# Kernel optimization log

Measured on AMD Instinct MI355X. Metric: run time of the kernel, lower is better.

## Reference

```python
import jax, jax.numpy as jnp
import numpy as np

RWKV_EPS = 1e-20
RWKV_K_CLAMP = 60.0

N, C, E = 25000, 128, 400000


def setup_inputs() -> dict:
    key = jax.random.key(0)
    ks = jax.random.split(key, 14)
    return {
        "x": jax.random.normal(ks[0], (N, C), jnp.float32),
        "prev_x": jax.random.normal(ks[1], (N, C), jnp.float32),
        "ah": jax.random.uniform(ks[2], (E, C), jnp.float32),
        "bh": jax.random.uniform(ks[3], (E, C), jnp.float32),
        "Wk": jax.random.normal(ks[4], (C, C), jnp.float32) / np.sqrt(C),
        "Wv": jax.random.normal(ks[5], (C, C), jnp.float32) / np.sqrt(C),
        "Wr": jax.random.normal(ks[6], (C, C), jnp.float32) / np.sqrt(C),
        "Wo": jax.random.normal(ks[7], (C, C), jnp.float32) / np.sqrt(C),
        "time_mix_k": jax.random.uniform(ks[8], (1, C), jnp.float32),
        "time_mix_v": jax.random.uniform(ks[9], (1, C), jnp.float32),
        "time_mix_r": jax.random.uniform(ks[10], (1, C), jnp.float32),
        "time_w": jax.random.uniform(ks[11], (1, C), jnp.float32),
        "s": jax.random.randint(ks[12], (E,), 0, N, jnp.int64),
        "t": jax.random.randint(ks[13], (E,), 0, N, jnp.int64),
        "i": 5,
        "T": 16,
    }


def reference(x, prev_x, ah, bh, Wk, Wv, Wr, Wo,
              time_mix_k, time_mix_v, time_mix_r, time_w, s, t, i, T):
    # time-shift mixing on node features [N, C]
    xk = x * time_mix_k + prev_x * (1.0 - time_mix_k)
    xv = x * time_mix_v + prev_x * (1.0 - time_mix_v)
    xr = x * time_mix_r + prev_x * (1.0 - time_mix_r)
    # torch Linear: y = x @ W.T ; gather to edges [E, C]
    k = (xk @ Wk.T)[s]
    v = (xv @ Wv.T)[t]
    r = jax.nn.sigmoid((xr @ Wr.T)[s])
    k = jnp.exp(jnp.minimum(k, RWKV_K_CLAMP))
    w = jnp.exp(-(T - i - 1) * time_w)  # [1, C] decay
    kv = w * (k * v)
    a = ah + kv
    b = bh + k
    wkv = a / (b + RWKV_EPS)
    out = (r * wkv) @ Wo.T  # [E, C]
    return out
```

## Files before the change

### kernel.cpp

```cpp
#include <hip/hip_runtime.h>

#define CDIM 128

typedef short short8 __attribute__((ext_vector_type(8)));
typedef float f32x4 __attribute__((ext_vector_type(4)));

__device__ __forceinline__ unsigned short f2bf(float f) {
  unsigned int u = __builtin_bit_cast(unsigned int, f);
  u += 0x7fffu + ((u >> 16) & 1u);
  return (unsigned short)(u >> 16);
}
__device__ __forceinline__ float bf2f(unsigned short b) {
  return __builtin_bit_cast(float, (unsigned int)b << 16);
}
__device__ __forceinline__ void split_bf(float v, unsigned short& h,
                                         unsigned short& l) {
  h = f2bf(v);
  l = f2bf(v - bf2f(h));
}


__global__ __launch_bounds__(256) void pack_w(
    const float* __restrict__ Wk, const float* __restrict__ Wv,
    const float* __restrict__ Wr, const float* __restrict__ Wo,
    unsigned short* __restrict__ wf) {
  const int f = blockIdx.x * 256 + threadIdx.x;
  const int m = f >> 12;
  const int idx = (f & 4095) * 4;
  const int e0 = idx & 7;
  const int l = (idx >> 3) & 63;
  const int nt = (idx >> 9) & 7;
  const int kt = idx >> 12;
  const float* W = (m == 0) ? Wk : (m == 1) ? Wv : (m == 2) ? Wr : Wo;
  const int j = nt * 16 + (l & 15);
  const int c = kt * 32 + (l >> 4) * 8 + e0;
  float4 v = *(const float4*)(W + j * CDIM + c);
  ushort4 h, lo;
  split_bf(v.x, h.x, lo.x);
  split_bf(v.y, h.y, lo.y);
  split_bf(v.z, h.z, lo.z);
  split_bf(v.w, h.w, lo.w);
  unsigned short* base = wf + m * 32768;
  *(ushort4*)(base + idx) = h;
  *(ushort4*)(base + 16384 + idx) = lo;
}


#define MFMA __builtin_amdgcn_mfma_f32_16x16x32_bf16

__device__ __forceinline__ void stage_w(unsigned short* Wl,
                                        const unsigned short* wsrc, int t) {
  const float4* src = (const float4*)wsrc;
  float4* dst = (float4*)Wl;
#pragma unroll
  for (int it = 0; it < 16; ++it) dst[it * 256 + t] = src[it * 256 + t];
}

__device__ __forceinline__ void mfma_all(const unsigned short* Wl,
                                         const short8 ahi[2][4],
                                         const short8 alo[2][4],
                                         f32x4 acc[2][8], int lane) {
#pragma unroll
  for (int kt = 0; kt < 4; ++kt) {
#pragma unroll
    for (int nt = 0; nt < 8; ++nt) {
      const int fo = ((kt * 8 + nt) * 64 + lane) * 8;
      short8 bhi = *(const short8*)(Wl + fo);
      short8 blo = *(const short8*)(Wl + 16384 + fo);
      acc[0][nt] = MFMA(ahi[0][kt], bhi, acc[0][nt], 0, 0, 0);
      acc[1][nt] = MFMA(ahi[1][kt], bhi, acc[1][nt], 0, 0, 0);
      acc[0][nt] = MFMA(alo[0][kt], bhi, acc[0][nt], 0, 0, 0);
      acc[1][nt] = MFMA(alo[1][kt], bhi, acc[1][nt], 0, 0, 0);
      acc[0][nt] = MFMA(ahi[0][kt], blo, acc[0][nt], 0, 0, 0);
      acc[1][nt] = MFMA(ahi[1][kt], blo, acc[1][nt], 0, 0, 0);
    }
  }
}

__global__ __launch_bounds__(256, 2) void node_mfma(
    const float* __restrict__ x, const float* __restrict__ px,
    const float* __restrict__ tmk, const float* __restrict__ tmv,
    const float* __restrict__ tmr, const unsigned short* __restrict__ wf,
    float* __restrict__ kvr, int N) {
  __shared__ alignas(16) unsigned short Wl[32768];
  const int t = threadIdx.x;
  const int m = blockIdx.y;
  stage_w(Wl, wf + m * 32768, t);
  const float* __restrict__ tm = (m == 0) ? tmk : (m == 1) ? tmv : tmr;
  const int lane = t & 63;
  const int w = t >> 6;
  const int lr = lane & 15, lg = lane >> 4;
  const int rbase = blockIdx.x * 128 + w * 32;

  short8 ahi[2][4], alo[2][4];
#pragma unroll
  for (int kt = 0; kt < 4; ++kt) {
    const int c0 = kt * 32 + lg * 8;
    float tmx[8];
    *(float4*)tmx = *(const float4*)(tm + c0);
    *(float4*)(tmx + 4) = *(const float4*)(tm + c0 + 4);
#pragma unroll
    for (int mt = 0; mt < 2; ++mt) {
      const int r = rbase + mt * 16 + lr;
      float xa[8], pa[8];
      if (r < N) {
        const float* xp = x + (size_t)r * CDIM + c0;
        const float* pp = px + (size_t)r * CDIM + c0;
        *(float4*)xa = *(const float4*)xp;
        *(float4*)(xa + 4) = *(const float4*)(xp + 4);
        *(float4*)pa = *(const float4*)pp;
        *(float4*)(pa + 4) = *(const float4*)(pp + 4);
      } else {
#pragma unroll
        for (int q = 0; q < 8; ++q) { xa[q] = 0.f; pa[q] = 0.f; }
      }
      short8 hv, lv;
#pragma unroll
      for (int q = 0; q < 8; ++q) {
        float xm = pa[q] + tmx[q] * (xa[q] - pa[q]);
        unsigned short hb, lb;
        split_bf(xm, hb, lb);
        hv[q] = (short)hb;
        lv[q] = (short)lb;
      }
      ahi[mt][kt] = hv;
      alo[mt][kt] = lv;
    }
  }
  __syncthreads();

  f32x4 acc[2][8];
#pragma unroll
  for (int mt = 0; mt < 2; ++mt)
#pragma unroll
    for (int nt = 0; nt < 8; ++nt) {
      f32x4 z = {0.f, 0.f, 0.f, 0.f};
      acc[mt][nt] = z;
    }
  mfma_all(Wl, ahi, alo, acc, lane);

  float* outb = kvr + (size_t)m * N * CDIM;
#pragma unroll
  for (int mt = 0; mt < 2; ++mt) {
    const int rb = rbase + mt * 16 + lg * 4;
#pragma unroll
    for (int nt = 0; nt < 8; ++nt) {
#pragma unroll
      for (int g = 0; g < 4; ++g) {
        const int r = rb + g;
        if (r < N) outb[(size_t)r * CDIM + nt * 16 + lr] = acc[mt][nt][g];
      }
    }
  }
}

__global__ __launch_bounds__(256, 2) void edge_mfma(
    const float* __restrict__ ah, const float* __restrict__ bh,
    const int* __restrict__ sidx, const int* __restrict__ tidx,
    const int* __restrict__ ip, const int* __restrict__ Tp,
    const float* __restrict__ time_w, const unsigned short* __restrict__ wf,
    const float* __restrict__ kvr, float* __restrict__ out, int N) {
  __shared__ alignas(16) unsigned short Wl[32768];
  const int t = threadIdx.x;
  stage_w(Wl, wf + 3 * 32768, t);
  const int lane = t & 63;
  const int w = t >> 6;
  const int lr = lane & 15, lg = lane >> 4;
  const size_t rbase = (size_t)blockIdx.x * 128 + w * 32;
  const float* __restrict__ Kb = kvr;
  const float* __restrict__ Vb = kvr + (size_t)N * CDIM;
  const float* __restrict__ Rb = kvr + 2 * (size_t)N * CDIM;
  const float dec = -(float)(Tp[0] - ip[0] - 1);

  const size_t er0 = rbase + lr, er1 = rbase + 16 + lr;
  const int s0 = sidx[er0], t0 = tidx[er0];
  const int s1 = sidx[er1], t1 = tidx[er1];

  short8 ahi[2][4], alo[2][4];
#pragma unroll
  for (int kt = 0; kt < 4; ++kt) {
    const int c0 = kt * 32 + lg * 8;
    float tww[8], wd[8];
    *(float4*)tww = *(const float4*)(time_w + c0);
    *(float4*)(tww + 4) = *(const float4*)(time_w + c0 + 4);
#pragma unroll
    for (int q = 0; q < 8; ++q) wd[q] = __expf(dec * tww[q]);
#pragma unroll
    for (int mt = 0; mt < 2; ++mt) {
      const size_t r = mt ? er1 : er0;
      const int se = mt ? s1 : s0;
      const int te = mt ? t1 : t0;
      float aa[8], bb[8], kk[8], vv[8], rr[8];
      {
        const float* p = ah + r * CDIM + c0;
        *(float4*)aa = *(const float4*)p;
        *(float4*)(aa + 4) = *(const float4*)(p + 4);
      }
      {
        const float* p = bh + r * CDIM + c0;
        *(float4*)bb = *(const float4*)p;
        *(float4*)(bb + 4) = *(const float4*)(p + 4);
      }
      {
        const float* p = Kb + (size_t)se * CDIM + c0;
        *(float4*)kk = *(const float4*)p;
        *(float4*)(kk + 4) = *(const float4*)(p + 4);
      }
      {
        const float* p = Vb + (size_t)te * CDIM + c0;
        *(float4*)vv = *(const float4*)p;
        *(float4*)(vv + 4) = *(const float4*)(p + 4);
      }
      {
        const float* p = Rb + (size_t)se * CDIM + c0;
        *(float4*)rr = *(const float4*)p;
        *(float4*)(rr + 4) = *(const float4*)(p + 4);
      }
      short8 hv, lv;
#pragma unroll
      for (int q = 0; q < 8; ++q) {
        float ke = __expf(fminf(kk[q], 60.0f));
        float sr = __builtin_amdgcn_rcpf(1.0f + __expf(-rr[q]));
        float p = sr * (aa[q] + wd[q] * ke * vv[q]) *
                  __builtin_amdgcn_rcpf(bb[q] + ke + 1e-20f);
        unsigned short hb, lb;
        split_bf(p, hb, lb);
        hv[q] = (short)hb;
        lv[q] = (short)lb;
      }
      ahi[mt][kt] = hv;
      alo[mt][kt] = lv;
    }
  }
  __syncthreads();

  f32x4 acc[2][8];
#pragma unroll
  for (int mt = 0; mt < 2; ++mt)
#pragma unroll
    for (int nt = 0; nt < 8; ++nt) {
      f32x4 z = {0.f, 0.f, 0.f, 0.f};
      acc[mt][nt] = z;
    }
  mfma_all(Wl, ahi, alo, acc, lane);

#pragma unroll
  for (int mt = 0; mt < 2; ++mt) {
    const size_t rb = rbase + mt * 16 + lg * 4;
#pragma unroll
    for (int nt = 0; nt < 8; ++nt) {
      float* o = out + rb * CDIM + nt * 16 + lr;
#pragma unroll
      for (int g = 0; g < 4; ++g) o[(size_t)g * CDIM] = acc[mt][nt][g];
    }
  }
}

extern "C" void kernel_launch(void* const* d_in, const int* in_sizes, int n_in,
                              void* d_out, int out_size, void* d_ws,
                              size_t ws_size, hipStream_t stream) {
  const float* x   = (const float*)d_in[0];
  const float* px  = (const float*)d_in[1];
  const float* ah  = (const float*)d_in[2];
  const float* bh  = (const float*)d_in[3];
  const float* Wk  = (const float*)d_in[4];
  const float* Wv  = (const float*)d_in[5];
  const float* Wr  = (const float*)d_in[6];
  const float* Wo  = (const float*)d_in[7];
  const float* tmk = (const float*)d_in[8];
  const float* tmv = (const float*)d_in[9];
  const float* tmr = (const float*)d_in[10];
  const float* tw  = (const float*)d_in[11];
  const int* sidx  = (const int*)d_in[12];
  const int* tidx  = (const int*)d_in[13];
  const int* ip    = (const int*)d_in[14];
  const int* Tp    = (const int*)d_in[15];
  const int N = in_sizes[0] / CDIM;
  const int E = in_sizes[2] / CDIM;

  unsigned short* wf = (unsigned short*)d_ws;
  float* kvr = (float*)(wf + 4 * 32768);
  float* out = (float*)d_out;

  pack_w<<<dim3(64), dim3(256), 0, stream>>>(Wk, Wv, Wr, Wo, wf);
  node_mfma<<<dim3((N + 127) / 128, 3), dim3(256), 0, stream>>>(
      x, px, tmk, tmv, tmr, wf, kvr, N);
  edge_mfma<<<dim3(E / 128), dim3(256), 0, stream>>>(
      ah, bh, sidx, tidx, ip, Tp, tw, wf, kvr, out, N);
}
```

Measured before the change: 576.9 us.

## Swap MFMA operands for row-contiguous vector stores and enlarge edge blocks

The MFMA operands are swapped so the weight fragment is the A operand and the activations are B. Each lane now holds four consecutive output columns of a single row, so results are written as 16-byte vector stores instead of scattered scalar stores. The edge kernel now uses 512-thread blocks covering 256 edges, which spreads the 64KB weight staging over twice as many edges, and it adds bounds clamping for edge counts that are not a multiple of the block size. Launch bounds are raised to 4 blocks per CU, which tightens register limits and may cause spills.

Measured after the change: 668.4 us. 15.9% more time.

```diff
diff --git a/kernel.cpp b/kernel.cpp
--- a/kernel.cpp
+++ b/kernel.cpp
@@ -45,39 +45,40 @@
   *(ushort4*)(base + 16384 + idx) = lo;
 }
 
-
 #define MFMA __builtin_amdgcn_mfma_f32_16x16x32_bf16
 
+template <int NTHR>
 __device__ __forceinline__ void stage_w(unsigned short* Wl,
                                         const unsigned short* wsrc, int t) {
   const float4* src = (const float4*)wsrc;
   float4* dst = (float4*)Wl;
 #pragma unroll
-  for (int it = 0; it < 16; ++it) dst[it * 256 + t] = src[it * 256 + t];
+  for (int it = 0; it < 4096 / NTHR; ++it)
+    dst[it * NTHR + t] = src[it * NTHR + t];
 }
 
 __device__ __forceinline__ void mfma_all(const unsigned short* Wl,
-                                         const short8 ahi[2][4],
-                                         const short8 alo[2][4],
+                                         const short8 phi[2][4],
+                                         const short8 plo[2][4],
                                          f32x4 acc[2][8], int lane) {
 #pragma unroll
   for (int kt = 0; kt < 4; ++kt) {
 #pragma unroll
-    for (int nt = 0; nt < 8; ++nt) {
-      const int fo = ((kt * 8 + nt) * 64 + lane) * 8;
-      short8 bhi = *(const short8*)(Wl + fo);
-      short8 blo = *(const short8*)(Wl + 16384 + fo);
-      acc[0][nt] = MFMA(ahi[0][kt], bhi, acc[0][nt], 0, 0, 0);
-      acc[1][nt] = MFMA(ahi[1][kt], bhi, acc[1][nt], 0, 0, 0);
-      acc[0][nt] = MFMA(alo[0][kt], bhi, acc[0][nt], 0, 0, 0);
-      acc[1][nt] = MFMA(alo[1][kt], bhi, acc[1][nt], 0, 0, 0);
-      acc[0][nt] = MFMA(ahi[0][kt], blo, acc[0][nt], 0, 0, 0);
-      acc[1][nt] = MFMA(ahi[1][kt], blo, acc[1][nt], 0, 0, 0);
-    }
-  }
-}
-
-__global__ __launch_bounds__(256, 2) void node_mfma(
+    for (int ft = 0; ft < 8; ++ft) {
+      const int fo = ((kt * 8 + ft) * 64 + lane) * 8;
+      short8 whi = *(const short8*)(Wl + fo);
+      short8 wlo = *(const short8*)(Wl + 16384 + fo);
+      acc[0][ft] = MFMA(whi, phi[0][kt], acc[0][ft], 0, 0, 0);
+      acc[1][ft] = MFMA(whi, phi[1][kt], acc[1][ft], 0, 0, 0);
+      acc[0][ft] = MFMA(whi, plo[0][kt], acc[0][ft], 0, 0, 0);
+      acc[1][ft] = MFMA(whi, plo[1][kt], acc[1][ft], 0, 0, 0);
+      acc[0][ft] = MFMA(wlo, phi[0][kt], acc[0][ft], 0, 0, 0);
+      acc[1][ft] = MFMA(wlo, phi[1][kt], acc[1][ft], 0, 0, 0);
+    }
+  }
+}
+
+__global__ __launch_bounds__(256, 4) void node_mfma(
     const float* __restrict__ x, const float* __restrict__ px,
     const float* __restrict__ tmk, const float* __restrict__ tmv,
     const float* __restrict__ tmr, const unsigned short* __restrict__ wf,
@@ -85,14 +86,14 @@
   __shared__ alignas(16) unsigned short Wl[32768];
   const int t = threadIdx.x;
   const int m = blockIdx.y;
-  stage_w(Wl, wf + m * 32768, t);
+  stage_w<256>(Wl, wf + m * 32768, t);
   const float* __restrict__ tm = (m == 0) ? tmk : (m == 1) ? tmv : tmr;
   const int lane = t & 63;
   const int w = t >> 6;
   const int lr = lane & 15, lg = lane >> 4;
   const int rbase = blockIdx.x * 128 + w * 32;
 
-  short8 ahi[2][4], alo[2][4];
+  short8 phi[2][4], plo[2][4];
 #pragma unroll
   for (int kt = 0; kt < 4; ++kt) {
     const int c0 = kt * 32 + lg * 8;
@@ -123,8 +124,8 @@
         hv[q] = (short)hb;
         lv[q] = (short)lb;
       }
-      ahi[mt][kt] = hv;
-      alo[mt][kt] = lv;
+      phi[mt][kt] = hv;
+      plo[mt][kt] = lv;
     }
   }
   __syncthreads();
@@ -133,50 +134,49 @@
 #pragma unroll
   for (int mt = 0; mt < 2; ++mt)
 #pragma unroll
-    for (int nt = 0; nt < 8; ++nt) {
+    for (int ft = 0; ft < 8; ++ft) {
       f32x4 z = {0.f, 0.f, 0.f, 0.f};
-      acc[mt][nt] = z;
-    }
-  mfma_all(Wl, ahi, alo, acc, lane);
+      acc[mt][ft] = z;
+    }
+  mfma_all(Wl, phi, plo, acc, lane);
 
   float* outb = kvr + (size_t)m * N * CDIM;
 #pragma unroll
   for (int mt = 0; mt < 2; ++mt) {
-    const int rb = rbase + mt * 16 + lg * 4;
-#pragma unroll
-    for (int nt = 0; nt < 8; ++nt) {
-#pragma unroll
-      for (int g = 0; g < 4; ++g) {
-        const int r = rb + g;
-        if (r < N) outb[(size_t)r * CDIM + nt * 16 + lr] = acc[mt][nt][g];
-      }
-    }
-  }
-}
-
-__global__ __launch_bounds__(256, 2) void edge_mfma(
+    const int r = rbase + mt * 16 + lr;
+    if (r < N) {
+#pragma unroll
+      for (int ft = 0; ft < 8; ++ft)
+        *(f32x4*)(outb + (size_t)r * CDIM + ft * 16 + lg * 4) = acc[mt][ft];
+    }
+  }
+}
+
+__global__ __launch_bounds__(512, 4) void edge_mfma(
     const float* __restrict__ ah, const float* __restrict__ bh,
     const int* __restrict__ sidx, const int* __restrict__ tidx,
     const int* __restrict__ ip, const int* __restrict__ Tp,
     const float* __restrict__ time_w, const unsigned short* __restrict__ wf,
-    const float* __restrict__ kvr, float* __restrict__ out, int N) {
+    const float* __restrict__ kvr, float* __restrict__ out, int N, int E) {
   __shared__ alignas(16) unsigned short Wl[32768];
   const int t = threadIdx.x;
-  stage_w(Wl, wf + 3 * 32768, t);
+  stage_w<512>(Wl, wf + 3 * 32768, t);
   const int lane = t & 63;
   const int w = t >> 6;
   const int lr = lane & 15, lg = lane >> 4;
-  const size_t rbase = (size_t)blockIdx.x * 128 + w * 32;
+  const size_t rbase = (size_t)blockIdx.x * 256 + w * 32;
   const float* __restrict__ Kb = kvr;
   const float* __restrict__ Vb = kvr + (size_t)N * CDIM;
   const float* __restrict__ Rb = kvr + 2 * (size_t)N * CDIM;
   const float dec = -(float)(Tp[0] - ip[0] - 1);
 
-  const size_t er0 = rbase + lr, er1 = rbase + 16 + lr;
-  const int s0 = sidx[er0], t0 = tidx[er0];
-  const int s1 = sidx[er1], t1 = tidx[er1];
-
-  short8 ahi[2][4], alo[2][4];
+  const size_t er0 = rbase + lr, er1 = er0 + 16;
+  const size_t ec0 = er0 < (size_t)E ? er0 : (size_t)(E - 1);
+  const size_t ec1 = er1 < (size_t)E ? er1 : (size_t)(E - 1);
+  const int s0 = sidx[ec0], t0 = tidx[ec0];
+  const int s1 = sidx[ec1], t1 = tidx[ec1];
+
+  short8 phi[2][4], plo[2][4];
 #pragma unroll
   for (int kt = 0; kt < 4; ++kt) {
     const int c0 = kt * 32 + lg * 8;
@@ -187,7 +187,7 @@
     for (int q = 0; q < 8; ++q) wd[q] = __expf(dec * tww[q]);
 #pragma unroll
     for (int mt = 0; mt < 2; ++mt) {
-      const size_t r = mt ? er1 : er0;
+      const size_t r = mt ? ec1 : ec0;
       const int se = mt ? s1 : s0;
       const int te = mt ? t1 : t0;
       float aa[8], bb[8], kk[8], vv[8], rr[8];
@@ -228,8 +228,8 @@
         hv[q] = (short)hb;
         lv[q] = (short)lb;
       }
-      ahi[mt][kt] = hv;
-      alo[mt][kt] = lv;
+      phi[mt][kt] = hv;
+      plo[mt][kt] = lv;
     }
   }
   __syncthreads();
@@ -238,20 +238,19 @@
 #pragma unroll
   for (int mt = 0; mt < 2; ++mt)
 #pragma unroll
-    for (int nt = 0; nt < 8; ++nt) {
+    for (int ft = 0; ft < 8; ++ft) {
       f32x4 z = {0.f, 0.f, 0.f, 0.f};
-      acc[mt][nt] = z;
-    }
-  mfma_all(Wl, ahi, alo, acc, lane);
+      acc[mt][ft] = z;
+    }
+  mfma_all(Wl, phi, plo, acc, lane);
 
 #pragma unroll
   for (int mt = 0; mt < 2; ++mt) {
-    const size_t rb = rbase + mt * 16 + lg * 4;
-#pragma unroll
-    for (int nt = 0; nt < 8; ++nt) {
-      float* o = out + rb * CDIM + nt * 16 + lr;
-#pragma unroll
-      for (int g = 0; g < 4; ++g) o[(size_t)g * CDIM] = acc[mt][nt][g];
+    const size_t e = rbase + mt * 16 + lr;
+    if (e < (size_t)E) {
+#pragma unroll
+      for (int ft = 0; ft < 8; ++ft)
+        *(f32x4*)(out + e * CDIM + ft * 16 + lg * 4) = acc[mt][ft];
     }
   }
 }
@@ -285,6 +284,6 @@
   pack_w<<<dim3(64), dim3(256), 0, stream>>>(Wk, Wv, Wr, Wo, wf);
   node_mfma<<<dim3((N + 127) / 128, 3), dim3(256), 0, stream>>>(
       x, px, tmk, tmv, tmr, wf, kvr, N);
-  edge_mfma<<<dim3(E / 128), dim3(256), 0, stream>>>(
-      ah, bh, sidx, tidx, ip, Tp, tw, wf, kvr, out, N);
-}
+  edge_mfma<<<dim3((E + 255) / 256), dim3(512), 0, stream>>>(
+      ah, bh, sidx, tidx, ip, Tp, tw, wf, kvr, out, N, E);
+}
```
